# Optimization experiments

Hardware: AMD Instinct MI355X
Metric: run time of the kernel (lower is better)

The kernel has to match this reference:

```python
import jax, jax.numpy as jnp
import numpy as np

GRID_SIZE = 5
SPLINE_ORDER = 3


def _haar_filters():
    # db1 (Haar) decomposition filters, matching wavelet.create_wavelet_filter:
    # dec_lo[::-1] = [s, s], dec_hi[::-1] = [s, -s]; rec filters are identical for Haar.
    s = np.float32(1.0 / np.sqrt(2.0))
    lo = np.array([s, s], np.float32)
    hi = np.array([s, -s], np.float32)
    # f = a.unsqueeze(0) * b.unsqueeze(1)  ->  f[p, q] = a[q] * b[p]
    def outer(a, b):
        return b[:, None] * a[None, :]
    dec = np.stack([outer(lo, lo), outer(lo, hi), outer(hi, lo), outer(hi, hi)], 0)  # (4,2,2): LL,LH,HL,HH
    return jnp.asarray(dec), jnp.asarray(dec)


def depthwise_conv5(x, w, b):
    # torch Conv2d(C, C, 5, padding='same', groups=C)
    y = jax.lax.conv_general_dilated(
        x, w, window_strides=(1, 1), padding=[(2, 2), (2, 2)],
        dimension_numbers=('NCHW', 'OIHW', 'NCHW'), feature_group_count=x.shape[1])
    return y + b[None, :, None, None]


def kan_linear(x, base_w, spline_w, scaler):
    # efficient-kan KANLinear: base SiLU linear + B-spline linear over last dim.
    in_f = x.shape[-1]
    out_f = base_w.shape[0]
    shp = x.shape
    xf = x.reshape(-1, in_f)                      # (N, in)
    h = 2.0 / GRID_SIZE                           # grid_range [-1, 1]
    grid_1d = jnp.arange(-SPLINE_ORDER, GRID_SIZE + SPLINE_ORDER + 1, dtype=xf.dtype) * h - 1.0
    grid = jnp.broadcast_to(grid_1d, (in_f, grid_1d.shape[0]))  # (in, G+2k+1)
    xe = xf[:, :, None]
    bases = ((xe >= grid[:, :-1]) & (xe < grid[:, 1:])).astype(xf.dtype)
    for k in range(1, SPLINE_ORDER + 1):
        bases = ((xe - grid[:, :-(k + 1)]) / (grid[:, k:-1] - grid[:, :-(k + 1)]) * bases[..., :-1]
                 + (grid[:, k + 1:] - xe) / (grid[:, k + 1:] - grid[:, 1:-k]) * bases[..., 1:])
    # bases: (N, in, G+k)
    base_out = jax.nn.silu(xf) @ base_w.T
    sw = spline_w * scaler[:, :, None]            # scaled_spline_weight (out, in, G+k)
    spline_out = jnp.einsum('nig,oig->no', bases, sw)
    return (base_out + spline_out).reshape(*shp[:-1], out_f)


def setup_inputs() -> dict:
    key = jax.random.key(0)
    ks = jax.random.split(key, 6)
    C, H, W, B = 32, 256, 256, 4
    in_f = C * 4  # 128
    return {
        'x': jax.random.normal(ks[0], (B, C, H, W), jnp.float32),
        'conv_w': jax.random.normal(ks[1], (C, 1, 5, 5), jnp.float32) * 0.2,
        'conv_b': jax.random.normal(ks[2], (C,), jnp.float32) * 0.02,
        'kan_base_w': jax.random.normal(ks[3], (in_f, in_f), jnp.float32) * (1.0 / np.sqrt(in_f)),
        'kan_spline_w': jax.random.normal(ks[4], (in_f, in_f, GRID_SIZE + SPLINE_ORDER), jnp.float32) * 0.1,
        'kan_spline_scaler': 1.0 + 0.1 * jax.random.normal(ks[5], (in_f, in_f), jnp.float32),
    }


def reference(x, conv_w, conv_b, kan_base_w, kan_spline_w, kan_spline_scaler):
    dec, rec = _haar_filters()
    b, c, hh, ww = x.shape
    # Level-1 skip: depthwise base_conv on full-res input
    skip = depthwise_conv5(x, conv_w, conv_b)
    # Haar wavelet transform (stride-2 non-overlapping 2x2 depthwise conv) via reshape+einsum
    x5 = x.reshape(b, c, hh // 2, 2, ww // 2, 2)
    wt = jnp.einsum('bcipjq,kpq->bckij', x5, dec)  # (b, c, 4, h/2, w/2)
    # Subband KAN over last (width) dim of 128 == in_channels*4 -> msi_kan branch
    z = kan_linear(wt, kan_base_w, kan_spline_w, kan_spline_scaler)
    # Inverse wavelet (stride-2 conv_transpose) via einsum scatter
    y = jnp.einsum('bckij,kpq->bcipjq', z, rec).reshape(b, c, hh, ww)
    return y + skip
```

## Files before the change

kernel.cpp:

```cpp
#include <hip/hip_runtime.h>
#include <hip/hip_bf16.h>

using f32x4 = __attribute__((ext_vector_type(4))) float;
using s16x8 = __attribute__((ext_vector_type(8))) short;
using u32x4 = __attribute__((ext_vector_type(4))) unsigned;

constexpr int Bn = 4, Cc = 32, Hh = 256, Ww = 256;
constexpr int H2 = 128, W2 = 128;
constexpr int NF = 128;
constexpr int KTOT = 1152;

__device__ __forceinline__ short f2bf(float f) {
    union { float f; unsigned u; } v; v.f = f;
    unsigned r = v.u + 0x7fffu + ((v.u >> 16) & 1u);
    return (short)(r >> 16);
}

__device__ __forceinline__ unsigned pk_bf16(float a, float b) {
    union { __hip_bfloat162 h; unsigned u; } c;
    c.h.x = __float2bfloat16(a);
    c.h.y = __float2bfloat16(b);
    return c.u;
}

__device__ __forceinline__ void gload_lds16(const void* g, void* l) {
    __builtin_amdgcn_global_load_lds(
        (const __attribute__((address_space(1))) unsigned*)g,
        (__attribute__((address_space(3))) unsigned*)l, 16, 0, 0);
}

__device__ __forceinline__ void window128(float wD, float wC, float wB, float wA,
                                          int ci, unsigned W[4]) {
    unsigned long long P = ((unsigned long long)pk_bf16(wB, wA) << 32)
                         | (unsigned long long)pk_bf16(wD, wC);
    int sh = ci * 16 - 48;
    unsigned long long sl = P << (sh & 63);
    unsigned long long sr = P >> ((-sh) & 63);
    unsigned long long lo = (sh < 0) ? sr : ((sh < 64) ? sl : 0ull);
    int shh = sh - 64;
    unsigned long long sl2 = P << (shh & 63);
    unsigned long long sr2 = P >> ((-shh) & 63);
    unsigned long long hi = (shh >= 0) ? sl2 : (((-shh) < 64) ? sr2 : 0ull);
    W[0] = (unsigned)lo; W[1] = (unsigned)(lo >> 32);
    W[2] = (unsigned)hi; W[3] = (unsigned)(hi >> 32);
}

__global__ __launch_bounds__(256) void k_wbuild(const float* __restrict__ base_w,
                                                const float* __restrict__ spline_w,
                                                const float* __restrict__ scaler,
                                                short* __restrict__ Bg) {
    int idx = blockIdx.x * 256 + threadIdx.x;
    int tile = idx >> 9;
    int r = idx & 511;
    int lane = r >> 3, q = r & 7;
    int ni = tile / 36; int rem = tile - ni * 36;
    int jg = rem / 9;   int ks = rem - jg * 9;
    int o = ni * 16 + (lane & 15);
    int kk = ks * 32 + (lane >> 4) * 8 + q;
    int g = kk >> 5, jl = kk & 31;
    int j = jg * 32 + jl;
    float v = (g == 0) ? base_w[o * NF + j]
                       : spline_w[(long)(o * NF + j) * 8 + (g - 1)] * scaler[o * NF + j];
    Bg[idx] = f2bf(v);
}

__global__ __launch_bounds__(256, 2) void k_fused(const float* __restrict__ x,
                                                  const float* __restrict__ cw,
                                                  const float* __restrict__ cb,
                                                  float* __restrict__ out,
                                                  const short* __restrict__ Bg) {
    __shared__ __align__(16) short Bsh[72 * 512];
    const int t = threadIdx.x;
    const int lane = t & 63;
    const int w = t >> 6;
    const int blk = blockIdx.x;
    const int plane = blk >> 2;
    const int band = blk & 3;
    const int i0 = band << 5;
    const int jg0 = blk & 3;
    const int il = lane & 15;
    const int fg = lane >> 4;

    const float sB = (w & 2) ? -1.f : 1.f;
    const float sC = (w & 1) ? -1.f : 1.f;
    const float sD = sB * sC;

    const float* xbase = x + (long)plane * Hh * Ww;
    const float* xr0a = xbase + (long)(2 * (i0 + il)) * Ww;
    const float* xr1a = xr0a + Ww;
    const float* xr0b = xbase + (long)(2 * (i0 + il + 16)) * Ww;
    const float* xr1b = xr0b + Ww;

    const int c = plane & 31;
    float cwr[25];
#pragma unroll
    for (int q = 0; q < 25; ++q) cwr[q] = cw[c * 25 + q];
    const float bias = cb[c];
    float* outp = out + (long)plane * Hh * Ww;
    const int qyg = w;

    f32x4 acc[2][8];
#pragma unroll
    for (int mi = 0; mi < 2; ++mi)
#pragma unroll
        for (int ni = 0; ni < 8; ++ni)
            acc[mi][ni] = (f32x4){0.f, 0.f, 0.f, 0.f};

    for (int j = 0; j < 4; ++j) {
        const int jg = (jg0 + j) & 3;
        const int cb2 = jg * 64 + fg * 16;

#pragma unroll
        for (int s = 0; s < 18; ++s) {
            int q = s * 4 + w;
            int ni = q / 9, ks = q - ni * 9;
            gload_lds16(&Bg[(long)(((ni * 4 + jg) * 9 + ks) << 9) + lane * 8],
                        &Bsh[q << 9]);
        }

        u32x4 afr[2][9];
#pragma unroll
        for (int mi = 0; mi < 2; ++mi) {
            const float* r0 = mi ? xr0b : xr0a;
            const float* r1 = mi ? xr1b : xr1a;
#pragma unroll
            for (int p = 0; p < 4; ++p) {
                f32x4 va = *(const f32x4*)(r0 + cb2 + 4 * p);
                f32x4 vb = *(const f32x4*)(r1 + cb2 + 4 * p);
                float vv[2];
                vv[0] = 0.5f * (va[0] + sB * va[1] + sC * vb[0] + sD * vb[1]);
                vv[1] = 0.5f * (va[2] + sB * va[3] + sC * vb[2] + sD * vb[3]);
                float sl2[2]; unsigned Wf[2][4];
#pragma unroll
                for (int e = 0; e < 2; ++e) {
                    float v = vv[e];
                    float ex = __builtin_amdgcn_exp2f(-1.442695040888963f * v);
                    sl2[e] = v * __builtin_amdgcn_rcpf(1.0f + ex);
                    float xs = __builtin_fmaf(v, 2.5f, 5.5f);
                    xs = fminf(fmaxf(xs, 0.0f), 10.999f);
                    float cf = floorf(xs);
                    float u = xs - cf;
                    int ci = (int)cf;
                    float u2 = u * u, u3 = u2 * u;
                    float wA = u3 * (1.f / 6.f);
                    float wB = (1.f + 3.f * u + 3.f * u2 - 3.f * u3) * (1.f / 6.f);
                    float wC = (4.f - 6.f * u2 + 3.f * u3) * (1.f / 6.f);
                    float um = 1.f - u;
                    float wD = um * um * um * (1.f / 6.f);
                    window128(wD, wC, wB, wA, ci, Wf[e]);
                }
                afr[mi][0][p] = pk_bf16(sl2[0], sl2[1]);
#pragma unroll
                for (int g = 1; g <= 8; ++g) {
                    int wq = (g - 1) >> 1;
                    unsigned sel = ((g - 1) & 1) ? 0x07060302u : 0x05040100u;
                    afr[mi][g][p] = __builtin_amdgcn_perm(Wf[1][wq], Wf[0][wq], sel);
                }
            }
        }

        __syncthreads();

        __builtin_amdgcn_s_setprio(1);
#pragma unroll
        for (int ks = 0; ks < 9; ++ks) {
            s16x8 bfr[8];
#pragma unroll
            for (int ni = 0; ni < 8; ++ni)
                bfr[ni] = *(const s16x8*)&Bsh[((ni * 9 + ks) << 9) + lane * 8];
#pragma unroll
            for (int mi = 0; mi < 2; ++mi) {
                s16x8 a = __builtin_bit_cast(s16x8, afr[mi][ks]);
#pragma unroll
                for (int ni = 0; ni < 8; ++ni)
                    acc[mi][ni] = __builtin_amdgcn_mfma_f32_16x16x32_bf16(
                        a, bfr[ni], acc[mi][ni], 0, 0, 0);
            }
        }
        __builtin_amdgcn_s_setprio(0);

#pragma unroll
        for (int qxh = 0; qxh < 2; ++qxh) {
            const int jq = qxh * 64 + lane;
            const float mlo = (jq >= 1) ? 1.f : 0.f;
            const float mhi = (jq <= 126) ? 1.f : 0.f;
            const int clo = (jq >= 1) ? (2 * jq - 2) : 0;
            const int cmid = 2 * jq;
            const int chi = (jq <= 126) ? (2 * jq + 2) : 252;
            float xv[6][6];
#pragma unroll
            for (int aa = 0; aa < 2; ++aa) {
                const int ql = qyg * 8 + 2 * j + aa;
                const int orow = 2 * (i0 + ql);
                const int rlo = (aa == 0) ? 0 : 4;
                if (aa) {
#pragma unroll
                    for (int r6 = 0; r6 < 4; ++r6)
#pragma unroll
                        for (int c6 = 0; c6 < 6; ++c6) xv[r6][c6] = xv[r6 + 2][c6];
                }
#pragma unroll
                for (int r6 = 0; r6 < 6; ++r6) {
                    if (r6 < rlo) continue;
                    int xr = orow - 2 + r6;
                    int xrc = min(max(xr, 0), Hh - 1);
                    float mrow = (xr >= 0 && xr < Hh) ? 1.f : 0.f;
                    const float* xrp = xbase + (long)xrc * Ww;
                    float2 lo = *(const float2*)(xrp + clo);
                    float2 mi2 = *(const float2*)(xrp + cmid);
                    float2 hi = *(const float2*)(xrp + chi);
                    float ml = mlo * mrow, mh = mhi * mrow;
                    xv[r6][0] = lo.x * ml;    xv[r6][1] = lo.y * ml;
                    xv[r6][2] = mi2.x * mrow; xv[r6][3] = mi2.y * mrow;
                    xv[r6][4] = hi.x * mh;    xv[r6][5] = hi.y * mh;
                }
                float s00 = bias, s01 = bias, s10 = bias, s11 = bias;
#pragma unroll
                for (int ky = 0; ky < 5; ++ky)
#pragma unroll
                    for (int kx = 0; kx < 5; ++kx) {
                        float wv = cwr[ky * 5 + kx];
                        s00 += wv * xv[ky][kx];
                        s01 += wv * xv[ky][kx + 1];
                        s10 += wv * xv[ky + 1][kx];
                        s11 += wv * xv[ky + 1][kx + 1];
                    }
                float* op = outp + (long)orow * Ww + 2 * jq;
                *(float2*)op        = make_float2(s00, s01);
                *(float2*)(op + Ww) = make_float2(s10, s11);
            }
        }

        __syncthreads();
    }

    constexpr int ZP = 132;
    float* zsh = (float*)Bsh;
#pragma unroll
    for (int mi = 0; mi < 2; ++mi)
#pragma unroll
        for (int rr = 0; rr < 4; ++rr)
#pragma unroll
            for (int ni = 0; ni < 8; ++ni)
                zsh[(w * 32 + mi * 16 + fg * 4 + rr) * ZP + ni * 16 + il]
                    = acc[mi][ni][rr];
    __syncthreads();

#pragma unroll
    for (int qxh = 0; qxh < 2; ++qxh) {
        const int jq = qxh * 64 + lane;
#pragma unroll
        for (int a = 0; a < 8; ++a) {
            const int ql = qyg * 8 + a;
            const int orow = 2 * (i0 + ql);
            float z0 = zsh[(ql) * ZP + jq];
            float z1 = zsh[(32 + ql) * ZP + jq];
            float z2 = zsh[(64 + ql) * ZP + jq];
            float z3 = zsh[(96 + ql) * ZP + jq];
            float y00 = 0.5f * (z0 + z1 + z2 + z3);
            float y01 = 0.5f * (z0 + z1 - z2 - z3);
            float y10 = 0.5f * (z0 - z1 + z2 - z3);
            float y11 = 0.5f * (z0 - z1 - z2 + z3);
            float* op = outp + (long)orow * Ww + 2 * jq;
            float2 p0 = *(float2*)op;
            float2 p1 = *(float2*)(op + Ww);
            p0.x += y00; p0.y += y01;
            p1.x += y10; p1.y += y11;
            *(float2*)op        = p0;
            *(float2*)(op + Ww) = p1;
        }
    }
}

extern "C" void kernel_launch(void* const* d_in, const int* in_sizes, int n_in,
                              void* d_out, int out_size, void* d_ws, size_t ws_size,
                              hipStream_t stream) {
    const float* x        = (const float*)d_in[0];
    const float* conv_w   = (const float*)d_in[1];
    const float* conv_b   = (const float*)d_in[2];
    const float* base_w   = (const float*)d_in[3];
    const float* spline_w = (const float*)d_in[4];
    const float* scaler   = (const float*)d_in[5];
    float* out = (float*)d_out;
    short* Bg  = (short*)d_ws;

    k_wbuild<<<(NF * KTOT) / 256, 256, 0, stream>>>(base_w, spline_w, scaler, Bg);
    k_fused<<<512, 256, 0, stream>>>(x, conv_w, conv_b, out, Bg);
}
```

Before: 67.20 us.

## Split output features across two blocks and fuse conv skip into final store

Each block now computes half of the 128 output features (64 columns), which doubles the grid to 1024 blocks and halves shared memory and accumulator registers. The depthwise 5x5 conv, which used to be interleaved with the GEMM loop and written to output before a read-modify-write add, is moved to the epilogue. There it is combined with the inverse Haar result and stored once, so the extra global read and write of the output disappears. The cost is that both column halves recompute the wavelet and spline A fragments, so that work is duplicated, and the conv no longer overlaps with the MFMA phase.

```diff
diff --git a/kernel.cpp b/kernel.cpp
--- a/kernel.cpp
+++ b/kernel.cpp
@@ -69,13 +69,14 @@
                                                   const float* __restrict__ cb,
                                                   float* __restrict__ out,
                                                   const short* __restrict__ Bg) {
-    __shared__ __align__(16) short Bsh[72 * 512];
+    __shared__ __align__(16) short Bsh[36 * 512];
     const int t = threadIdx.x;
     const int lane = t & 63;
     const int w = t >> 6;
     const int blk = blockIdx.x;
-    const int plane = blk >> 2;
-    const int band = blk & 3;
+    const int nc = blk & 1;
+    const int band = (blk >> 1) & 3;
+    const int plane = blk >> 3;
     const int i0 = band << 5;
     const int jg0 = blk & 3;
     const int il = lane & 15;
@@ -91,19 +92,11 @@
     const float* xr0b = xbase + (long)(2 * (i0 + il + 16)) * Ww;
     const float* xr1b = xr0b + Ww;
 
-    const int c = plane & 31;
-    float cwr[25];
-#pragma unroll
-    for (int q = 0; q < 25; ++q) cwr[q] = cw[c * 25 + q];
-    const float bias = cb[c];
-    float* outp = out + (long)plane * Hh * Ww;
-    const int qyg = w;
-
-    f32x4 acc[2][8];
+    f32x4 acc[2][4];
 #pragma unroll
     for (int mi = 0; mi < 2; ++mi)
 #pragma unroll
-        for (int ni = 0; ni < 8; ++ni)
+        for (int ni = 0; ni < 4; ++ni)
             acc[mi][ni] = (f32x4){0.f, 0.f, 0.f, 0.f};
 
     for (int j = 0; j < 4; ++j) {
@@ -111,10 +104,11 @@
         const int cb2 = jg * 64 + fg * 16;
 
 #pragma unroll
-        for (int s = 0; s < 18; ++s) {
+        for (int s = 0; s < 9; ++s) {
             int q = s * 4 + w;
-            int ni = q / 9, ks = q - ni * 9;
-            gload_lds16(&Bg[(long)(((ni * 4 + jg) * 9 + ks) << 9) + lane * 8],
+            int nl = q / 9, ks = q - nl * 9;
+            int ng = nc * 4 + nl;
+            gload_lds16(&Bg[(long)(((ng * 4 + jg) * 9 + ks) << 9) + lane * 8],
                         &Bsh[q << 9]);
         }
 
@@ -164,111 +158,98 @@
         __builtin_amdgcn_s_setprio(1);
 #pragma unroll
         for (int ks = 0; ks < 9; ++ks) {
-            s16x8 bfr[8];
-#pragma unroll
-            for (int ni = 0; ni < 8; ++ni)
-                bfr[ni] = *(const s16x8*)&Bsh[((ni * 9 + ks) << 9) + lane * 8];
+            s16x8 bfr[4];
+#pragma unroll
+            for (int nl = 0; nl < 4; ++nl)
+                bfr[nl] = *(const s16x8*)&Bsh[((nl * 9 + ks) << 9) + lane * 8];
 #pragma unroll
             for (int mi = 0; mi < 2; ++mi) {
                 s16x8 a = __builtin_bit_cast(s16x8, afr[mi][ks]);
 #pragma unroll
-                for (int ni = 0; ni < 8; ++ni)
-                    acc[mi][ni] = __builtin_amdgcn_mfma_f32_16x16x32_bf16(
-                        a, bfr[ni], acc[mi][ni], 0, 0, 0);
+                for (int nl = 0; nl < 4; ++nl)
+                    acc[mi][nl] = __builtin_amdgcn_mfma_f32_16x16x32_bf16(
+                        a, bfr[nl], acc[mi][nl], 0, 0, 0);
             }
         }
         __builtin_amdgcn_s_setprio(0);
-
-#pragma unroll
-        for (int qxh = 0; qxh < 2; ++qxh) {
-            const int jq = qxh * 64 + lane;
-            const float mlo = (jq >= 1) ? 1.f : 0.f;
-            const float mhi = (jq <= 126) ? 1.f : 0.f;
-            const int clo = (jq >= 1) ? (2 * jq - 2) : 0;
-            const int cmid = 2 * jq;
-            const int chi = (jq <= 126) ? (2 * jq + 2) : 252;
-            float xv[6][6];
-#pragma unroll
-            for (int aa = 0; aa < 2; ++aa) {
-                const int ql = qyg * 8 + 2 * j + aa;
-                const int orow = 2 * (i0 + ql);
-                const int rlo = (aa == 0) ? 0 : 4;
-                if (aa) {
-#pragma unroll
-                    for (int r6 = 0; r6 < 4; ++r6)
-#pragma unroll
-                        for (int c6 = 0; c6 < 6; ++c6) xv[r6][c6] = xv[r6 + 2][c6];
-                }
-#pragma unroll
-                for (int r6 = 0; r6 < 6; ++r6) {
-                    if (r6 < rlo) continue;
-                    int xr = orow - 2 + r6;
-                    int xrc = min(max(xr, 0), Hh - 1);
-                    float mrow = (xr >= 0 && xr < Hh) ? 1.f : 0.f;
-                    const float* xrp = xbase + (long)xrc * Ww;
-                    float2 lo = *(const float2*)(xrp + clo);
-                    float2 mi2 = *(const float2*)(xrp + cmid);
-                    float2 hi = *(const float2*)(xrp + chi);
-                    float ml = mlo * mrow, mh = mhi * mrow;
-                    xv[r6][0] = lo.x * ml;    xv[r6][1] = lo.y * ml;
-                    xv[r6][2] = mi2.x * mrow; xv[r6][3] = mi2.y * mrow;
-                    xv[r6][4] = hi.x * mh;    xv[r6][5] = hi.y * mh;
-                }
-                float s00 = bias, s01 = bias, s10 = bias, s11 = bias;
-#pragma unroll
-                for (int ky = 0; ky < 5; ++ky)
-#pragma unroll
-                    for (int kx = 0; kx < 5; ++kx) {
-                        float wv = cwr[ky * 5 + kx];
-                        s00 += wv * xv[ky][kx];
-                        s01 += wv * xv[ky][kx + 1];
-                        s10 += wv * xv[ky + 1][kx];
-                        s11 += wv * xv[ky + 1][kx + 1];
-                    }
-                float* op = outp + (long)orow * Ww + 2 * jq;
-                *(float2*)op        = make_float2(s00, s01);
-                *(float2*)(op + Ww) = make_float2(s10, s11);
-            }
-        }
-
         __syncthreads();
     }
 
-    constexpr int ZP = 132;
+    constexpr int ZP = 66;
     float* zsh = (float*)Bsh;
 #pragma unroll
     for (int mi = 0; mi < 2; ++mi)
 #pragma unroll
         for (int rr = 0; rr < 4; ++rr)
 #pragma unroll
-            for (int ni = 0; ni < 8; ++ni)
-                zsh[(w * 32 + mi * 16 + fg * 4 + rr) * ZP + ni * 16 + il]
-                    = acc[mi][ni][rr];
+            for (int nl = 0; nl < 4; ++nl)
+                zsh[(w * 32 + mi * 16 + fg * 4 + rr) * ZP + nl * 16 + il]
+                    = acc[mi][nl][rr];
     __syncthreads();
 
-#pragma unroll
-    for (int qxh = 0; qxh < 2; ++qxh) {
-        const int jq = qxh * 64 + lane;
-#pragma unroll
-        for (int a = 0; a < 8; ++a) {
-            const int ql = qyg * 8 + a;
-            const int orow = 2 * (i0 + ql);
-            float z0 = zsh[(ql) * ZP + jq];
-            float z1 = zsh[(32 + ql) * ZP + jq];
-            float z2 = zsh[(64 + ql) * ZP + jq];
-            float z3 = zsh[(96 + ql) * ZP + jq];
-            float y00 = 0.5f * (z0 + z1 + z2 + z3);
-            float y01 = 0.5f * (z0 + z1 - z2 - z3);
-            float y10 = 0.5f * (z0 - z1 + z2 - z3);
-            float y11 = 0.5f * (z0 - z1 - z2 + z3);
-            float* op = outp + (long)orow * Ww + 2 * jq;
-            float2 p0 = *(float2*)op;
-            float2 p1 = *(float2*)(op + Ww);
-            p0.x += y00; p0.y += y01;
-            p1.x += y10; p1.y += y11;
-            *(float2*)op        = p0;
-            *(float2*)(op + Ww) = p1;
-        }
+    const int c = plane & 31;
+    float cwr[25];
+#pragma unroll
+    for (int q = 0; q < 25; ++q) cwr[q] = cw[c * 25 + q];
+    const float bias = cb[c];
+    float* outp = out + (long)plane * Hh * Ww;
+
+    const int jglob = nc * 64 + lane;
+    const float mlo = (jglob >= 1) ? 1.f : 0.f;
+    const float mhi = (jglob <= 126) ? 1.f : 0.f;
+    const int clo = (jglob >= 1) ? (2 * jglob - 2) : 0;
+    const int cmid = 2 * jglob;
+    const int chi = (jglob <= 126) ? (2 * jglob + 2) : 252;
+
+    float xv[6][6];
+#pragma unroll
+    for (int a = 0; a < 8; ++a) {
+        const int ql = w * 8 + a;
+        const int orow = 2 * (i0 + ql);
+        const int rlo = (a == 0) ? 0 : 4;
+        if (a) {
+#pragma unroll
+            for (int r6 = 0; r6 < 4; ++r6)
+#pragma unroll
+                for (int c6 = 0; c6 < 6; ++c6) xv[r6][c6] = xv[r6 + 2][c6];
+        }
+#pragma unroll
+        for (int r6 = 0; r6 < 6; ++r6) {
+            if (r6 < rlo) continue;
+            int xr = orow - 2 + r6;
+            int xrc = min(max(xr, 0), Hh - 1);
+            float mrow = (xr >= 0 && xr < Hh) ? 1.f : 0.f;
+            const float* xrp = xbase + (long)xrc * Ww;
+            float2 lo = *(const float2*)(xrp + clo);
+            float2 mi2 = *(const float2*)(xrp + cmid);
+            float2 hi = *(const float2*)(xrp + chi);
+            float ml = mlo * mrow, mh = mhi * mrow;
+            xv[r6][0] = lo.x * ml;    xv[r6][1] = lo.y * ml;
+            xv[r6][2] = mi2.x * mrow; xv[r6][3] = mi2.y * mrow;
+            xv[r6][4] = hi.x * mh;    xv[r6][5] = hi.y * mh;
+        }
+        float z0 = zsh[(ql) * ZP + lane];
+        float z1 = zsh[(32 + ql) * ZP + lane];
+        float z2 = zsh[(64 + ql) * ZP + lane];
+        float z3 = zsh[(96 + ql) * ZP + lane];
+        float y00 = 0.5f * (z0 + z1 + z2 + z3);
+        float y01 = 0.5f * (z0 + z1 - z2 - z3);
+        float y10 = 0.5f * (z0 - z1 + z2 - z3);
+        float y11 = 0.5f * (z0 - z1 - z2 + z3);
+        float s00 = bias, s01 = bias, s10 = bias, s11 = bias;
+#pragma unroll
+        for (int ky = 0; ky < 5; ++ky)
+#pragma unroll
+            for (int kx = 0; kx < 5; ++kx) {
+                float wv = cwr[ky * 5 + kx];
+                s00 += wv * xv[ky][kx];
+                s01 += wv * xv[ky][kx + 1];
+                s10 += wv * xv[ky + 1][kx];
+                s11 += wv * xv[ky + 1][kx + 1];
+            }
+        float* op = outp + (long)orow * Ww + 2 * jglob;
+        *(float2*)op        = make_float2(s00 + y00, s01 + y01);
+        *(float2*)(op + Ww) = make_float2(s10 + y10, s11 + y11);
     }
 }
 
@@ -285,5 +266,5 @@
     short* Bg  = (short*)d_ws;
 
     k_wbuild<<<(NF * KTOT) / 256, 256, 0, stream>>>(base_w, spline_w, scaler, Bg);
-    k_fused<<<512, 256, 0, stream>>>(x, conv_w, conv_b, out, Bg);
-}
+    k_fused<<<1024, 256, 0, stream>>>(x, conv_w, conv_b, out, Bg);
+}
```

Measured after the change: 75.32 us. 1.12x slower.

## Use 8 waves per block and fuse conv epilogue with inverse wavelet write

Applied to the files above, without the earlier changes.

Doubles the block to 512 threads so each wave handles one 16-row M half instead of two, which halves accumulator and A-fragment registers per wave. The depthwise 5x5 conv is moved out of the per-j GEMM loop into the final epilogue, where it is summed with the inverse-Haar result and written once. This removes the read-modify-write of the output. The trade-off is that the conv no longer overlaps with MFMA work inside the loop, and each block now has more waves contending for LDS and barriers.

```diff
diff --git a/kernel.cpp b/kernel.cpp
--- a/kernel.cpp
+++ b/kernel.cpp
@@ -64,7 +64,7 @@
     Bg[idx] = f2bf(v);
 }
 
-__global__ __launch_bounds__(256, 2) void k_fused(const float* __restrict__ x,
+__global__ __launch_bounds__(512, 4) void k_fused(const float* __restrict__ x,
                                                   const float* __restrict__ cw,
                                                   const float* __restrict__ cb,
                                                   float* __restrict__ out,
@@ -72,7 +72,9 @@
     __shared__ __align__(16) short Bsh[72 * 512];
     const int t = threadIdx.x;
     const int lane = t & 63;
-    const int w = t >> 6;
+    const int wv = t >> 6;
+    const int kcomp = wv & 3;
+    const int mih = wv >> 2;
     const int blk = blockIdx.x;
     const int plane = blk >> 2;
     const int band = blk & 3;
@@ -81,15 +83,93 @@
     const int il = lane & 15;
     const int fg = lane >> 4;
 
-    const float sB = (w & 2) ? -1.f : 1.f;
-    const float sC = (w & 1) ? -1.f : 1.f;
+    const float sB = (kcomp & 2) ? -1.f : 1.f;
+    const float sC = (kcomp & 1) ? -1.f : 1.f;
     const float sD = sB * sC;
 
     const float* xbase = x + (long)plane * Hh * Ww;
-    const float* xr0a = xbase + (long)(2 * (i0 + il)) * Ww;
-    const float* xr1a = xr0a + Ww;
-    const float* xr0b = xbase + (long)(2 * (i0 + il + 16)) * Ww;
-    const float* xr1b = xr0b + Ww;
+    const float* xr0 = xbase + (long)(2 * (i0 + mih * 16 + il)) * Ww;
+    const float* xr1 = xr0 + Ww;
+
+    f32x4 acc[8];
+#pragma unroll
+    for (int ni = 0; ni < 8; ++ni)
+        acc[ni] = (f32x4){0.f, 0.f, 0.f, 0.f};
+
+    for (int j = 0; j < 4; ++j) {
+        const int jg = (jg0 + j) & 3;
+        const int cb2 = jg * 64 + fg * 16;
+
+#pragma unroll
+        for (int s = 0; s < 9; ++s) {
+            int q = s * 8 + wv;
+            int nl = q / 9, ks = q - nl * 9;
+            gload_lds16(&Bg[(long)(((nl * 4 + jg) * 9 + ks) << 9) + lane * 8],
+                        &Bsh[q << 9]);
+        }
+
+        u32x4 afr[9];
+#pragma unroll
+        for (int p = 0; p < 4; ++p) {
+            f32x4 va = *(const f32x4*)(xr0 + cb2 + 4 * p);
+            f32x4 vb = *(const f32x4*)(xr1 + cb2 + 4 * p);
+            float vv[2];
+            vv[0] = 0.5f * (va[0] + sB * va[1] + sC * vb[0] + sD * vb[1]);
+            vv[1] = 0.5f * (va[2] + sB * va[3] + sC * vb[2] + sD * vb[3]);
+            float sl2[2]; unsigned Wf[2][4];
+#pragma unroll
+            for (int e = 0; e < 2; ++e) {
+                float v = vv[e];
+                float ex = __builtin_amdgcn_exp2f(-1.442695040888963f * v);
+                sl2[e] = v * __builtin_amdgcn_rcpf(1.0f + ex);
+                float xs = __builtin_fmaf(v, 2.5f, 5.5f);
+                xs = fminf(fmaxf(xs, 0.0f), 10.999f);
+                float cf = floorf(xs);
+                float u = xs - cf;
+                int ci = (int)cf;
+                float u2 = u * u, u3 = u2 * u;
+                float wA = u3 * (1.f / 6.f);
+                float wB = (1.f + 3.f * u + 3.f * u2 - 3.f * u3) * (1.f / 6.f);
+                float wC = (4.f - 6.f * u2 + 3.f * u3) * (1.f / 6.f);
+                float um = 1.f - u;
+                float wD = um * um * um * (1.f / 6.f);
+                window128(wD, wC, wB, wA, ci, Wf[e]);
+            }
+            afr[0][p] = pk_bf16(sl2[0], sl2[1]);
+#pragma unroll
+            for (int g = 1; g <= 8; ++g) {
+                int wq = (g - 1) >> 1;
+                unsigned sel = ((g - 1) & 1) ? 0x07060302u : 0x05040100u;
+                afr[g][p] = __builtin_amdgcn_perm(Wf[1][wq], Wf[0][wq], sel);
+            }
+        }
+
+        __syncthreads();
+
+#pragma unroll
+        for (int ks = 0; ks < 9; ++ks) {
+            s16x8 bfr[8];
+#pragma unroll
+            for (int ni = 0; ni < 8; ++ni)
+                bfr[ni] = *(const s16x8*)&Bsh[((ni * 9 + ks) << 9) + lane * 8];
+            s16x8 a = __builtin_bit_cast(s16x8, afr[ks]);
+#pragma unroll
+            for (int ni = 0; ni < 8; ++ni)
+                acc[ni] = __builtin_amdgcn_mfma_f32_16x16x32_bf16(
+                    a, bfr[ni], acc[ni], 0, 0, 0);
+        }
+        __syncthreads();
+    }
+
+    constexpr int ZP = 132;
+    float* zsh = (float*)Bsh;
+#pragma unroll
+    for (int rr = 0; rr < 4; ++rr)
+#pragma unroll
+        for (int ni = 0; ni < 8; ++ni)
+            zsh[(kcomp * 32 + mih * 16 + fg * 4 + rr) * ZP + ni * 16 + il]
+                = acc[ni][rr];
+    __syncthreads();
 
     const int c = plane & 31;
     float cwr[25];
@@ -97,162 +177,42 @@
     for (int q = 0; q < 25; ++q) cwr[q] = cw[c * 25 + q];
     const float bias = cb[c];
     float* outp = out + (long)plane * Hh * Ww;
-    const int qyg = w;
-
-    f32x4 acc[2][8];
-#pragma unroll
-    for (int mi = 0; mi < 2; ++mi)
-#pragma unroll
-        for (int ni = 0; ni < 8; ++ni)
-            acc[mi][ni] = (f32x4){0.f, 0.f, 0.f, 0.f};
-
-    for (int j = 0; j < 4; ++j) {
-        const int jg = (jg0 + j) & 3;
-        const int cb2 = jg * 64 + fg * 16;
-
-#pragma unroll
-        for (int s = 0; s < 18; ++s) {
-            int q = s * 4 + w;
-            int ni = q / 9, ks = q - ni * 9;
-            gload_lds16(&Bg[(long)(((ni * 4 + jg) * 9 + ks) << 9) + lane * 8],
-                        &Bsh[q << 9]);
-        }
-
-        u32x4 afr[2][9];
-#pragma unroll
-        for (int mi = 0; mi < 2; ++mi) {
-            const float* r0 = mi ? xr0b : xr0a;
-            const float* r1 = mi ? xr1b : xr1a;
-#pragma unroll
-            for (int p = 0; p < 4; ++p) {
-                f32x4 va = *(const f32x4*)(r0 + cb2 + 4 * p);
-                f32x4 vb = *(const f32x4*)(r1 + cb2 + 4 * p);
-                float vv[2];
-                vv[0] = 0.5f * (va[0] + sB * va[1] + sC * vb[0] + sD * vb[1]);
-                vv[1] = 0.5f * (va[2] + sB * va[3] + sC * vb[2] + sD * vb[3]);
-                float sl2[2]; unsigned Wf[2][4];
-#pragma unroll
-                for (int e = 0; e < 2; ++e) {
-                    float v = vv[e];
-                    float ex = __builtin_amdgcn_exp2f(-1.442695040888963f * v);
-                    sl2[e] = v * __builtin_amdgcn_rcpf(1.0f + ex);
-                    float xs = __builtin_fmaf(v, 2.5f, 5.5f);
-                    xs = fminf(fmaxf(xs, 0.0f), 10.999f);
-                    float cf = floorf(xs);
-                    float u = xs - cf;
-                    int ci = (int)cf;
-                    float u2 = u * u, u3 = u2 * u;
-                    float wA = u3 * (1.f / 6.f);
-                    float wB = (1.f + 3.f * u + 3.f * u2 - 3.f * u3) * (1.f / 6.f);
-                    float wC = (4.f - 6.f * u2 + 3.f * u3) * (1.f / 6.f);
-                    float um = 1.f - u;
-                    float wD = um * um * um * (1.f / 6.f);
-                    window128(wD, wC, wB, wA, ci, Wf[e]);
-                }
-                afr[mi][0][p] = pk_bf16(sl2[0], sl2[1]);
-#pragma unroll
-                for (int g = 1; g <= 8; ++g) {
-                    int wq = (g - 1) >> 1;
-                    unsigned sel = ((g - 1) & 1) ? 0x07060302u : 0x05040100u;
-                    afr[mi][g][p] = __builtin_amdgcn_perm(Wf[1][wq], Wf[0][wq], sel);
-                }
-            }
-        }
-
-        __syncthreads();
-
-        __builtin_amdgcn_s_setprio(1);
-#pragma unroll
-        for (int ks = 0; ks < 9; ++ks) {
-            s16x8 bfr[8];
-#pragma unroll
-            for (int ni = 0; ni < 8; ++ni)
-                bfr[ni] = *(const s16x8*)&Bsh[((ni * 9 + ks) << 9) + lane * 8];
-#pragma unroll
-            for (int mi = 0; mi < 2; ++mi) {
-                s16x8 a = __builtin_bit_cast(s16x8, afr[mi][ks]);
-#pragma unroll
-                for (int ni = 0; ni < 8; ++ni)
-                    acc[mi][ni] = __builtin_amdgcn_mfma_f32_16x16x32_bf16(
-                        a, bfr[ni], acc[mi][ni], 0, 0, 0);
-            }
-        }
-        __builtin_amdgcn_s_setprio(0);
-
-#pragma unroll
-        for (int qxh = 0; qxh < 2; ++qxh) {
-            const int jq = qxh * 64 + lane;
-            const float mlo = (jq >= 1) ? 1.f : 0.f;
-            const float mhi = (jq <= 126) ? 1.f : 0.f;
-            const int clo = (jq >= 1) ? (2 * jq - 2) : 0;
-            const int cmid = 2 * jq;
-            const int chi = (jq <= 126) ? (2 * jq + 2) : 252;
-            float xv[6][6];
-#pragma unroll
-            for (int aa = 0; aa < 2; ++aa) {
-                const int ql = qyg * 8 + 2 * j + aa;
-                const int orow = 2 * (i0 + ql);
-                const int rlo = (aa == 0) ? 0 : 4;
-                if (aa) {
-#pragma unroll
-                    for (int r6 = 0; r6 < 4; ++r6)
-#pragma unroll
-                        for (int c6 = 0; c6 < 6; ++c6) xv[r6][c6] = xv[r6 + 2][c6];
-                }
-#pragma unroll
-                for (int r6 = 0; r6 < 6; ++r6) {
-                    if (r6 < rlo) continue;
-                    int xr = orow - 2 + r6;
-                    int xrc = min(max(xr, 0), Hh - 1);
-                    float mrow = (xr >= 0 && xr < Hh) ? 1.f : 0.f;
-                    const float* xrp = xbase + (long)xrc * Ww;
-                    float2 lo = *(const float2*)(xrp + clo);
-                    float2 mi2 = *(const float2*)(xrp + cmid);
-                    float2 hi = *(const float2*)(xrp + chi);
-                    float ml = mlo * mrow, mh = mhi * mrow;
-                    xv[r6][0] = lo.x * ml;    xv[r6][1] = lo.y * ml;
-                    xv[r6][2] = mi2.x * mrow; xv[r6][3] = mi2.y * mrow;
-                    xv[r6][4] = hi.x * mh;    xv[r6][5] = hi.y * mh;
-                }
-                float s00 = bias, s01 = bias, s10 = bias, s11 = bias;
-#pragma unroll
-                for (int ky = 0; ky < 5; ++ky)
-#pragma unroll
-                    for (int kx = 0; kx < 5; ++kx) {
-                        float wv = cwr[ky * 5 + kx];
-                        s00 += wv * xv[ky][kx];
-                        s01 += wv * xv[ky][kx + 1];
-                        s10 += wv * xv[ky + 1][kx];
-                        s11 += wv * xv[ky + 1][kx + 1];
-                    }
-                float* op = outp + (long)orow * Ww + 2 * jq;
-                *(float2*)op        = make_float2(s00, s01);
-                *(float2*)(op + Ww) = make_float2(s10, s11);
-            }
-        }
-
-        __syncthreads();
-    }
-
-    constexpr int ZP = 132;
-    float* zsh = (float*)Bsh;
-#pragma unroll
-    for (int mi = 0; mi < 2; ++mi)
-#pragma unroll
-        for (int rr = 0; rr < 4; ++rr)
-#pragma unroll
-            for (int ni = 0; ni < 8; ++ni)
-                zsh[(w * 32 + mi * 16 + fg * 4 + rr) * ZP + ni * 16 + il]
-                    = acc[mi][ni][rr];
-    __syncthreads();
 
 #pragma unroll
     for (int qxh = 0; qxh < 2; ++qxh) {
         const int jq = qxh * 64 + lane;
-#pragma unroll
-        for (int a = 0; a < 8; ++a) {
-            const int ql = qyg * 8 + a;
+        const float mlo = (jq >= 1) ? 1.f : 0.f;
+        const float mhi = (jq <= 126) ? 1.f : 0.f;
+        const int clo = (jq >= 1) ? (2 * jq - 2) : 0;
+        const int cmid = 2 * jq;
+        const int chi = (jq <= 126) ? (2 * jq + 2) : 252;
+        float xv[6][6];
+#pragma unroll
+        for (int a = 0; a < 4; ++a) {
+            const int ql = wv * 4 + a;
             const int orow = 2 * (i0 + ql);
+            const int rlo = (a == 0) ? 0 : 4;
+            if (a) {
+#pragma unroll
+                for (int r6 = 0; r6 < 4; ++r6)
+#pragma unroll
+                    for (int c6 = 0; c6 < 6; ++c6) xv[r6][c6] = xv[r6 + 2][c6];
+            }
+#pragma unroll
+            for (int r6 = 0; r6 < 6; ++r6) {
+                if (r6 < rlo) continue;
+                int xr = orow - 2 + r6;
+                int xrc = min(max(xr, 0), Hh - 1);
+                float mrow = (xr >= 0 && xr < Hh) ? 1.f : 0.f;
+                const float* xrp = xbase + (long)xrc * Ww;
+                float2 lo = *(const float2*)(xrp + clo);
+                float2 mi2 = *(const float2*)(xrp + cmid);
+                float2 hi = *(const float2*)(xrp + chi);
+                float ml = mlo * mrow, mh = mhi * mrow;
+                xv[r6][0] = lo.x * ml;    xv[r6][1] = lo.y * ml;
+                xv[r6][2] = mi2.x * mrow; xv[r6][3] = mi2.y * mrow;
+                xv[r6][4] = hi.x * mh;    xv[r6][5] = hi.y * mh;
+            }
             float z0 = zsh[(ql) * ZP + jq];
             float z1 = zsh[(32 + ql) * ZP + jq];
             float z2 = zsh[(64 + ql) * ZP + jq];
@@ -261,13 +221,20 @@
             float y01 = 0.5f * (z0 + z1 - z2 - z3);
             float y10 = 0.5f * (z0 - z1 + z2 - z3);
             float y11 = 0.5f * (z0 - z1 - z2 + z3);
+            float s00 = bias, s01 = bias, s10 = bias, s11 = bias;
+#pragma unroll
+            for (int ky = 0; ky < 5; ++ky)
+#pragma unroll
+                for (int kx = 0; kx < 5; ++kx) {
+                    float wv2 = cwr[ky * 5 + kx];
+                    s00 += wv2 * xv[ky][kx];
+                    s01 += wv2 * xv[ky][kx + 1];
+                    s10 += wv2 * xv[ky + 1][kx];
+                    s11 += wv2 * xv[ky + 1][kx + 1];
+                }
             float* op = outp + (long)orow * Ww + 2 * jq;
-            float2 p0 = *(float2*)op;
-            float2 p1 = *(float2*)(op + Ww);
-            p0.x += y00; p0.y += y01;
-            p1.x += y10; p1.y += y11;
-            *(float2*)op        = p0;
-            *(float2*)(op + Ww) = p1;
+            *(float2*)op        = make_float2(s00 + y00, s01 + y01);
+            *(float2*)(op + Ww) = make_float2(s10 + y10, s11 + y11);
         }
     }
 }
@@ -285,5 +252,5 @@
     short* Bg  = (short*)d_ws;
 
     k_wbuild<<<(NF * KTOT) / 256, 256, 0, stream>>>(base_w, spline_w, scaler, Bg);
-    k_fused<<<512, 256, 0, stream>>>(x, conv_w, conv_b, out, Bg);
-}
+    k_fused<<<512, 512, 0, stream>>>(x, conv_w, conv_b, out, Bg);
+}
```

Result: faster. 54.51 us (median of 2 runs) (-18.9%).
